# Kernel tuning notes

Measured on AMD Instinct MI355X. Metric: run time of the kernel, lower is better.

Reference implementation:

```python
import jax, jax.numpy as jnp
import numpy as np
import math

DIM_MODEL = 1024
N_HEAD = 16
NUM_NEURON = 64
MAX_LEN = 2048
B, S = 4, 2048


def setup_inputs() -> dict:
    key = jax.random.key(0)
    ks = jax.random.split(key, 11)
    d, p = DIM_MODEL, N_HEAD * NUM_NEURON
    sc_in = 1.0 / math.sqrt(d)
    sc_p = 1.0 / math.sqrt(p)
    return {
        "q": jax.random.normal(ks[0], (B, S, d), jnp.float32),
        "k": jax.random.normal(ks[1], (B, S, d), jnp.float32),
        "v": jax.random.normal(ks[2], (B, S, d), jnp.float32),
        "Wq": jax.random.normal(ks[3], (d, p), jnp.float32) * sc_in,
        "bq": jnp.zeros((p,), jnp.float32),
        "Wk": jax.random.normal(ks[4], (d, p), jnp.float32) * sc_in,
        "bk": jnp.zeros((p,), jnp.float32),
        "Wv": jax.random.normal(ks[5], (d, p), jnp.float32) * sc_in,
        "bv": jnp.zeros((p,), jnp.float32),
        "Wf": jax.random.normal(ks[6], (p, d), jnp.float32) * sc_p,
        "bf": jnp.zeros((d,), jnp.float32),
    }


def _split_heads(x):  # [B,S,H*Dh] -> [B,H,S,Dh]
    b, s, _ = x.shape
    return x.reshape(b, s, N_HEAD, NUM_NEURON).transpose(0, 2, 1, 3)


def reference(q, k, v, Wq, bq, Wk, bk, Wv, bv, Wf, bf):
    qh = _split_heads(q @ Wq + bq)
    kh = _split_heads(k @ Wk + bk)
    vh = _split_heads(v @ Wv + bv)
    # NOTE: original scales by 1/sqrt(max_len), not 1/sqrt(head_dim)
    scores = jnp.einsum("bhqd,bhkd->bhqk", qh, kh) / math.sqrt(MAX_LEN)
    s = scores.shape[-1]
    causal = jnp.tril(jnp.ones((s, s), bool))  # [S,S]
    scores = jnp.where(causal[None, None], scores, -jnp.inf)
    attn = jax.nn.softmax(scores, axis=-1)
    out = jnp.einsum("bhqk,bhkd->bhqd", attn, vh)  # [B,H,S,Dh]
    c = out.transpose(0, 2, 1, 3).reshape(out.shape[0], out.shape[2], N_HEAD * NUM_NEURON)
    return c @ Wf + bf
```

## Files before the change

### kernel.cpp

```cpp
#include <hip/hip_runtime.h>
#include <stdint.h>

#define DMODEL 1024
#define NHEAD 16
#define DH 64
#define BB 4
#define SS 2048
#define MROWS (BB * SS)

typedef __bf16 bfx8 __attribute__((ext_vector_type(8)));
typedef float f32x4 __attribute__((ext_vector_type(4)));
typedef float fvec4 __attribute__((ext_vector_type(4)));
typedef int i32x4 __attribute__((ext_vector_type(4)));
typedef unsigned short u16x8 __attribute__((ext_vector_type(8)));
typedef unsigned short u16x4 __attribute__((ext_vector_type(4)));

__device__ __forceinline__ unsigned short f2bf(float f) {
    union { float f; unsigned int u; } v; v.f = f;
    unsigned int r = v.u + 0x7FFFu + ((v.u >> 16) & 1u);
    return (unsigned short)(r >> 16);
}

__device__ __forceinline__ unsigned int cvtpk(float lo, float hi) {
    unsigned int r;
    asm("v_cvt_pk_bf16_f32 %0, %1, %2" : "=v"(r) : "v"(lo), "v"(hi));
    return r;
}

typedef __attribute__((address_space(1))) const void gas_t;
typedef __attribute__((address_space(3))) void las_t;
__device__ __forceinline__ void gload_lds16(const void* g, void* l) {
    __builtin_amdgcn_global_load_lds((gas_t*)g, (las_t*)l, 16, 0, 0);
}

__device__ __forceinline__ int sigma_k(int i) {
    return (i & 0x20) | ((i & 0x0C) << 1) | ((i & 0x10) >> 2) | (i & 3);
}

__global__ void cvt3_kernel(const float* __restrict__ s0, const float* __restrict__ s1,
                            const float* __restrict__ s2,
                            unsigned short* __restrict__ d0, unsigned short* __restrict__ d1,
                            unsigned short* __restrict__ d2, int n8)
{
    const float* s = (blockIdx.y == 0) ? s0 : (blockIdx.y == 1) ? s1 : s2;
    unsigned short* d = (blockIdx.y == 0) ? d0 : (blockIdx.y == 1) ? d1 : d2;
    int i = blockIdx.x * blockDim.x + threadIdx.x;
    if (i >= n8) return;
    fvec4 a = *reinterpret_cast<const fvec4*>(&s[(size_t)i * 8]);
    fvec4 b = *reinterpret_cast<const fvec4*>(&s[(size_t)i * 8 + 4]);
    u16x8 o;
    #pragma unroll
    for (int j = 0; j < 4; ++j) { o[j] = f2bf(a[j]); o[j + 4] = f2bf(b[j]); }
    *reinterpret_cast<u16x8*>(&d[(size_t)i * 8]) = o;
}

__global__ void transpose_cvt3_kernel(const float* __restrict__ W0, unsigned short* __restrict__ T0,
                                      const float* __restrict__ W1, unsigned short* __restrict__ T1,
                                      const float* __restrict__ W2, unsigned short* __restrict__ T2)
{
    const float* W = (blockIdx.z == 0) ? W0 : (blockIdx.z == 1) ? W1 : W2;
    unsigned short* Wt = (blockIdx.z == 0) ? T0 : (blockIdx.z == 1) ? T1 : T2;
    __shared__ unsigned short t[64][72];
    const int tid = threadIdx.x;
    const int r0 = blockIdx.y * 64, c0 = blockIdx.x * 64;
    #pragma unroll
    for (int i = 0; i < 4; ++i) {
        int idx = tid + i * 256;
        int r = idx >> 4, c4 = idx & 15;
        fvec4 v = *reinterpret_cast<const fvec4*>(&W[(size_t)(r0 + r) * DMODEL + c0 + c4 * 4]);
        #pragma unroll
        for (int j = 0; j < 4; ++j) t[c4 * 4 + j][r] = f2bf(v[j]);
    }
    __syncthreads();
    #pragma unroll
    for (int i = 0; i < 2; ++i) {
        int idx = tid + i * 256;
        int r = idx >> 3, c8 = idx & 7;
        u16x8 v = *reinterpret_cast<const u16x8*>(&t[r][c8 * 8]);
        *reinterpret_cast<u16x8*>(&Wt[(size_t)(c0 + r) * DMODEL + r0 + c8 * 8]) = v;
    }
}

struct GArg {
    const unsigned short* A;
    const unsigned short* Bt;
    const float* bias;
    void* O;
    float osc;
    int mode;
};

__global__ __launch_bounds__(256, 2)
void gemm_kernel(GArg g0, GArg g1, int M, int N, int K)
{
    const GArg g = blockIdx.z ? g1 : g0;
    __shared__ unsigned short sA[128 * 64];
    __shared__ unsigned short sB[128 * 64];
    const int tid  = threadIdx.x;
    const int lane = tid & 63;
    const int wave = tid >> 6;
    const int wm = (wave >> 1) * 64, wn = (wave & 1) * 64;
    const int m0 = blockIdx.x * 128, n0 = blockIdx.y * 128;
    const int lr = lane & 15;
    const int lg = lane >> 4;

    f32x4 acc[4][4] = {};

    for (int kk0 = 0; kk0 < K; kk0 += 64) {
        __syncthreads();
        #pragma unroll
        for (int i = 0; i < 4; ++i) {
            int c = tid + i * 256;
            int row = c >> 3, col8 = c & 7;
            gload_lds16(&g.A[(size_t)(m0 + row) * K + kk0 + col8 * 8], &sA[c * 8]);
        }
        #pragma unroll
        for (int i = 0; i < 4; ++i) {
            int c = tid + i * 256;
            int row = c >> 3, col8 = c & 7;
            gload_lds16(&g.Bt[(size_t)(n0 + row) * K + kk0 + col8 * 8], &sB[c * 8]);
        }
        __syncthreads();

        bfx8 af[4][2], bfr[4][2];
        #pragma unroll
        for (int m = 0; m < 4; ++m)
            #pragma unroll
            for (int kk = 0; kk < 2; ++kk)
                af[m][kk] = *reinterpret_cast<const bfx8*>(
                    &sA[(wm + m * 16 + lr) * 64 + kk * 32 + lg * 8]);
        #pragma unroll
        for (int n = 0; n < 4; ++n)
            #pragma unroll
            for (int kk = 0; kk < 2; ++kk)
                bfr[n][kk] = *reinterpret_cast<const bfx8*>(
                    &sB[(wn + n * 16 + lr) * 64 + kk * 32 + lg * 8]);
        #pragma unroll
        for (int kk = 0; kk < 2; ++kk)
            #pragma unroll
            for (int m = 0; m < 4; ++m)
                #pragma unroll
                for (int n = 0; n < 4; ++n)
                    acc[m][n] = __builtin_amdgcn_mfma_f32_16x16x32_bf16(
                        af[m][kk], bfr[n][kk], acc[m][n], 0, 0, 0);
    }

    #pragma unroll
    for (int n = 0; n < 4; ++n) {
        int col = n0 + wn + n * 16 + lr;
        float bv = g.bias[col];
        #pragma unroll
        for (int m = 0; m < 4; ++m) {
            int rowb = m0 + wm + m * 16 + lg * 4;
            float val[4];
            #pragma unroll
            for (int r = 0; r < 4; ++r) val[r] = (acc[m][n][r] + bv) * g.osc;
            if (g.mode == 0) {
                #pragma unroll
                for (int r = 0; r < 4; ++r)
                    ((unsigned short*)g.O)[(size_t)(rowb + r) * N + col] = f2bf(val[r]);
            } else if (g.mode == 2) {
                #pragma unroll
                for (int r = 0; r < 4; ++r)
                    ((float*)g.O)[(size_t)(rowb + r) * N + col] = val[r];
            } else {
                int bq = rowb >> 11, s = rowb & 2047;
                int hh = col >> 6, d = col & 63;
                u16x4 pk;
                #pragma unroll
                for (int r = 0; r < 4; ++r) pk[r] = f2bf(val[r]);
                size_t idx = ((size_t)(bq * 16 + hh) * 64 + d) * 2048 + s;
                *reinterpret_cast<u16x4*>(&((unsigned short*)g.O)[idx]) = pk;
            }
        }
    }
}

__global__ __launch_bounds__(256, 2)
void attn_kernel(const unsigned short* __restrict__ Q,
                 const unsigned short* __restrict__ K,
                 const unsigned short* __restrict__ Vt,
                 unsigned short* __restrict__ C)
{
    __shared__ unsigned short sK[64][72];
    __shared__ unsigned short sVt[64][72];

    const int tid  = threadIdx.x;
    const int lane = tid & 63;
    const int wave = tid >> 6;
    const int lr = lane & 15, lg = lane >> 4;
    const int bh = blockIdx.x;
    const int qt = (int)(gridDim.y - 1) - (int)blockIdx.y;
    const int b = bh >> 4, h = bh & 15;
    const int q0 = qt * 128;
    const size_t rowbase = (size_t)b * SS;
    const int hcol = h * DH;

    const int srow = tid >> 3, sc8 = tid & 7;
    const int sig0 = sigma_k(srow), sig1 = sigma_k(srow + 32);

    bfx8 aq[2][2];
    #pragma unroll
    for (int m = 0; m < 2; ++m) {
        int qr = q0 + wave * 32 + m * 16 + lr;
        const unsigned short* p = &Q[(rowbase + qr) * DMODEL + hcol + lg * 8];
        aq[m][0] = *reinterpret_cast<const bfx8*>(p);
        aq[m][1] = *reinterpret_cast<const bfx8*>(p + 32);
    }

    float m_run[2] = {0.f, 0.f};
    f32x4 l4[2] = {};
    f32x4 acc_o[2][4] = {};
    bool mz = true;
    const int qmax_wave = q0 + wave * 32 + 31;
    const int ntiles = 2 * qt + 2;

    for (int t = 0; t < ntiles; ++t) {
        const int k0 = t * 64;
        __syncthreads();
        *reinterpret_cast<u16x8*>(&sK[srow][sc8 * 8]) =
            *reinterpret_cast<const u16x8*>(
                &K[(rowbase + k0 + sig0) * DMODEL + hcol + sc8 * 8]);
        *reinterpret_cast<u16x8*>(&sK[srow + 32][sc8 * 8]) =
            *reinterpret_cast<const u16x8*>(
                &K[(rowbase + k0 + sig1) * DMODEL + hcol + sc8 * 8]);
        *reinterpret_cast<u16x8*>(&sVt[srow][sc8 * 8]) =
            *reinterpret_cast<const u16x8*>(
                &Vt[((size_t)bh * DH + srow) * SS + k0 + sc8 * 8]);
        *reinterpret_cast<u16x8*>(&sVt[srow + 32][sc8 * 8]) =
            *reinterpret_cast<const u16x8*>(
                &Vt[((size_t)bh * DH + srow + 32) * SS + k0 + sc8 * 8]);
        __syncthreads();
        if (k0 > qmax_wave) continue;

        f32x4 sc[2][4];
        __builtin_amdgcn_s_setprio(1);
        #pragma unroll
        for (int nf = 0; nf < 4; ++nf) {
            bfx8 ak0 = *reinterpret_cast<const bfx8*>(&sK[nf * 16 + lr][lg * 8]);
            bfx8 ak1 = *reinterpret_cast<const bfx8*>(&sK[nf * 16 + lr][32 + lg * 8]);
            #pragma unroll
            for (int m = 0; m < 2; ++m) {
                f32x4 s = {0.f, 0.f, 0.f, 0.f};
                s = __builtin_amdgcn_mfma_f32_16x16x32_bf16(ak0, aq[m][0], s, 0, 0, 0);
                s = __builtin_amdgcn_mfma_f32_16x16x32_bf16(ak1, aq[m][1], s, 0, 0, 0);
                sc[m][nf] = s;
            }
        }
        __builtin_amdgcn_s_setprio(0);
        #pragma unroll
        for (int m = 0; m < 2; ++m) {
            if (k0 + 63 > q0 + wave * 32 + m * 16) {
                int qrow = q0 + wave * 32 + m * 16 + lr;
                #pragma unroll
                for (int nf = 0; nf < 4; ++nf) {
                    int kb = k0 + ((nf >> 1) << 5) + (lg << 3) + ((nf & 1) << 2);
                    #pragma unroll
                    for (int r = 0; r < 4; ++r)
                        if (kb + r > qrow) sc[m][nf][r] = -3.0e38f;
                }
            }
        }
        f32x4 mx4 = sc[0][0];
        #pragma unroll
        for (int m = 0; m < 2; ++m)
            #pragma unroll
            for (int nf = 0; nf < 4; ++nf)
                #pragma unroll
                for (int r = 0; r < 4; ++r) mx4[r] = fmaxf(mx4[r], sc[m][nf][r]);
        float pmax = fmaxf(fmaxf(mx4[0], mx4[1]), fmaxf(mx4[2], mx4[3]));
        if (mz && __all(pmax <= 8.0f)) {
            #pragma unroll
            for (int m = 0; m < 2; ++m)
                #pragma unroll
                for (int nf = 0; nf < 4; ++nf) {
                    #pragma unroll
                    for (int r = 0; r < 4; ++r)
                        sc[m][nf][r] = __builtin_exp2f(sc[m][nf][r]);
                    l4[m] += sc[m][nf];
                }
        } else {
            mz = false;
            #pragma unroll
            for (int m = 0; m < 2; ++m) {
                float mx = -3.0e38f;
                #pragma unroll
                for (int nf = 0; nf < 4; ++nf)
                    #pragma unroll
                    for (int r = 0; r < 4; ++r) mx = fmaxf(mx, sc[m][nf][r]);
                mx = fmaxf(mx, __shfl_xor(mx, 16, 64));
                mx = fmaxf(mx, __shfl_xor(mx, 32, 64));
                float mnew = fmaxf(m_run[m], mx);
                float fs = __builtin_exp2f(m_run[m] - mnew);
                m_run[m] = mnew;
                f32x4 ps = {0.f, 0.f, 0.f, 0.f};
                #pragma unroll
                for (int nf = 0; nf < 4; ++nf) {
                    #pragma unroll
                    for (int r = 0; r < 4; ++r)
                        sc[m][nf][r] = __builtin_exp2f(sc[m][nf][r] - mnew);
                    ps += sc[m][nf];
                }
                #pragma unroll
                for (int r = 0; r < 4; ++r) l4[m][r] = l4[m][r] * fs + ps[r];
                #pragma unroll
                for (int r = 0; r < 4; ++r) {
                    float fsa = __shfl(fs, lg * 4 + r, 64);
                    #pragma unroll
                    for (int d = 0; d < 4; ++d) acc_o[m][d][r] *= fsa;
                }
            }
        }
        #pragma unroll
        for (int h2 = 0; h2 < 2; ++h2) {
            union { i32x4 i; bfx8 b; } pa[2];
            #pragma unroll
            for (int m = 0; m < 2; ++m) {
                pa[m].i[0] = cvtpk(sc[m][2 * h2][0],     sc[m][2 * h2][1]);
                pa[m].i[1] = cvtpk(sc[m][2 * h2][2],     sc[m][2 * h2][3]);
                pa[m].i[2] = cvtpk(sc[m][2 * h2 + 1][0], sc[m][2 * h2 + 1][1]);
                pa[m].i[3] = cvtpk(sc[m][2 * h2 + 1][2], sc[m][2 * h2 + 1][3]);
            }
            __builtin_amdgcn_s_setprio(1);
            #pragma unroll
            for (int d = 0; d < 4; ++d) {
                bfx8 bv0 = *reinterpret_cast<const bfx8*>(&sVt[d * 16 + lr][h2 * 32 + lg * 8]);
                acc_o[0][d] = __builtin_amdgcn_mfma_f32_16x16x32_bf16(pa[0].b, bv0, acc_o[0][d], 0, 0, 0);
                acc_o[1][d] = __builtin_amdgcn_mfma_f32_16x16x32_bf16(pa[1].b, bv0, acc_o[1][d], 0, 0, 0);
            }
            __builtin_amdgcn_s_setprio(0);
        }
    }

    #pragma unroll
    for (int m = 0; m < 2; ++m) {
        float l = (l4[m][0] + l4[m][1]) + (l4[m][2] + l4[m][3]);
        l += __shfl_xor(l, 16, 64);
        l += __shfl_xor(l, 32, 64);
        float linv = 1.0f / l;
        float linva[4];
        #pragma unroll
        for (int r = 0; r < 4; ++r) linva[r] = __shfl(linv, lg * 4 + r, 64);
        const int qrb = q0 + wave * 32 + m * 16 + lg * 4;
        #pragma unroll
        for (int d = 0; d < 4; ++d) {
            int col = hcol + d * 16 + lr;
            #pragma unroll
            for (int r = 0; r < 4; ++r)
                C[(rowbase + qrb + r) * DMODEL + col] = f2bf(acc_o[m][d][r] * linva[r]);
        }
    }
}

extern "C" void kernel_launch(void* const* d_in, const int* in_sizes, int n_in,
                              void* d_out, int out_size, void* d_ws, size_t ws_size,
                              hipStream_t stream)
{
    const float* q  = (const float*)d_in[0];
    const float* k  = (const float*)d_in[1];
    const float* v  = (const float*)d_in[2];
    const float* Wq = (const float*)d_in[3];
    const float* bq = (const float*)d_in[4];
    const float* Wk = (const float*)d_in[5];
    const float* bk = (const float*)d_in[6];
    const float* Wv = (const float*)d_in[7];
    const float* bv = (const float*)d_in[8];
    const float* Wf = (const float*)d_in[9];
    const float* bf = (const float*)d_in[10];

    unsigned short* ws = (unsigned short*)d_ws;
    const size_t SZ = (size_t)MROWS * DMODEL;
    unsigned short* ws0 = ws;
    unsigned short* ws1 = ws + SZ;
    unsigned short* ws2 = ws + 2 * SZ;
    unsigned short* ws3 = ws + 3 * SZ;

    unsigned short* scr = (unsigned short*)d_out;
    unsigned short* WqT = scr;
    unsigned short* WkT = scr + 1048576;
    unsigned short* WvT = scr + 2097152;
    unsigned short* Qb  = scr + 4194304;

    const float qscale = 0.02209708691207961f * 1.44269504088896341f;

    const int n8 = (int)(SZ / 8);
    cvt3_kernel<<<dim3((n8 + 255) / 256, 3), 256, 0, stream>>>(q, k, v, ws0, ws1, ws2, n8);

    transpose_cvt3_kernel<<<dim3(16, 16, 3), 256, 0, stream>>>(Wq, WqT, Wk, WkT, Wv, WvT);

    {
        GArg gq{ws0, WqT, bq, Qb,  qscale, 0};
        GArg gk{ws1, WkT, bk, ws3, 1.0f,   0};
        gemm_kernel<<<dim3(64, 8, 2), 256, 0, stream>>>(gq, gk, MROWS, DMODEL, DMODEL);
    }
    {
        GArg gv{ws2, WvT, bv, ws0, 1.0f, 3};
        gemm_kernel<<<dim3(64, 8, 1), 256, 0, stream>>>(gv, gv, MROWS, DMODEL, DMODEL);
    }
    transpose_cvt3_kernel<<<dim3(16, 16, 1), 256, 0, stream>>>(Wf, ws2, Wf, ws2, Wf, ws2);

    attn_kernel<<<dim3(BB * NHEAD, SS / 128), 256, 0, stream>>>(Qb, ws3, ws0, ws1);

    {
        GArg gf{ws1, ws2, bf, (float*)d_out, 1.0f, 2};
        gemm_kernel<<<dim3(64, 8, 1), 256, 0, stream>>>(gf, gf, MROWS, DMODEL, DMODEL);
    }
}
```

Before: 212.8 us.

## Prefetch next K/V tile into registers and XOR-swizzle shared memory layout

The attention kernel now loads the next K and Vt tile from global memory into registers while the current tile is being computed, then stores them to shared memory at the top of the next iteration. This is meant to hide global load latency behind the MFMA work. The padded shared arrays are replaced with unpadded 64x64 arrays using an XOR swizzle on the 16-byte chunk index, to avoid bank conflicts without the padding. It costs extra registers for the prefetch buffers, which could reduce occupancy under launch_bounds(256,2).

```diff
diff --git a/kernel.cpp b/kernel.cpp
--- a/kernel.cpp
+++ b/kernel.cpp
@@ -182,8 +182,8 @@
                  const unsigned short* __restrict__ Vt,
                  unsigned short* __restrict__ C)
 {
-    __shared__ unsigned short sK[64][72];
-    __shared__ unsigned short sVt[64][72];
+    __shared__ unsigned short sK[64 * 64];
+    __shared__ unsigned short sV[64 * 64];
 
     const int tid  = threadIdx.x;
     const int lane = tid & 63;
@@ -198,6 +198,9 @@
 
     const int srow = tid >> 3, sc8 = tid & 7;
     const int sig0 = sigma_k(srow), sig1 = sigma_k(srow + 32);
+    const int woff0 = srow * 64 + ((sc8 ^ (srow & 7)) * 8);
+    const int woff1 = (srow + 32) * 64 + ((sc8 ^ (srow & 7)) * 8);
+    const int p0 = lg ^ (lr & 7);
 
     bfx8 aq[2][2];
     #pragma unroll
@@ -215,30 +218,38 @@
     const int qmax_wave = q0 + wave * 32 + 31;
     const int ntiles = 2 * qt + 2;
 
+    u16x8 rk0, rk1, rv0, rv1;
+    {
+        rk0 = *reinterpret_cast<const u16x8*>(&K[(rowbase + 0 + sig0) * DMODEL + hcol + sc8 * 8]);
+        rk1 = *reinterpret_cast<const u16x8*>(&K[(rowbase + 0 + sig1) * DMODEL + hcol + sc8 * 8]);
+        rv0 = *reinterpret_cast<const u16x8*>(&Vt[((size_t)bh * DH + srow) * SS + 0 + sc8 * 8]);
+        rv1 = *reinterpret_cast<const u16x8*>(&Vt[((size_t)bh * DH + srow + 32) * SS + 0 + sc8 * 8]);
+    }
+
     for (int t = 0; t < ntiles; ++t) {
+        __syncthreads();
+        *reinterpret_cast<u16x8*>(&sK[woff0]) = rk0;
+        *reinterpret_cast<u16x8*>(&sK[woff1]) = rk1;
+        *reinterpret_cast<u16x8*>(&sV[woff0]) = rv0;
+        *reinterpret_cast<u16x8*>(&sV[woff1]) = rv1;
+        __syncthreads();
+        if (t + 1 < ntiles) {
+            const int kk = (t + 1) * 64;
+            rk0 = *reinterpret_cast<const u16x8*>(&K[(rowbase + kk + sig0) * DMODEL + hcol + sc8 * 8]);
+            rk1 = *reinterpret_cast<const u16x8*>(&K[(rowbase + kk + sig1) * DMODEL + hcol + sc8 * 8]);
+            rv0 = *reinterpret_cast<const u16x8*>(&Vt[((size_t)bh * DH + srow) * SS + kk + sc8 * 8]);
+            rv1 = *reinterpret_cast<const u16x8*>(&Vt[((size_t)bh * DH + srow + 32) * SS + kk + sc8 * 8]);
+        }
         const int k0 = t * 64;
-        __syncthreads();
-        *reinterpret_cast<u16x8*>(&sK[srow][sc8 * 8]) =
-            *reinterpret_cast<const u16x8*>(
-                &K[(rowbase + k0 + sig0) * DMODEL + hcol + sc8 * 8]);
-        *reinterpret_cast<u16x8*>(&sK[srow + 32][sc8 * 8]) =
-            *reinterpret_cast<const u16x8*>(
-                &K[(rowbase + k0 + sig1) * DMODEL + hcol + sc8 * 8]);
-        *reinterpret_cast<u16x8*>(&sVt[srow][sc8 * 8]) =
-            *reinterpret_cast<const u16x8*>(
-                &Vt[((size_t)bh * DH + srow) * SS + k0 + sc8 * 8]);
-        *reinterpret_cast<u16x8*>(&sVt[srow + 32][sc8 * 8]) =
-            *reinterpret_cast<const u16x8*>(
-                &Vt[((size_t)bh * DH + srow + 32) * SS + k0 + sc8 * 8]);
-        __syncthreads();
         if (k0 > qmax_wave) continue;
 
         f32x4 sc[2][4];
         __builtin_amdgcn_s_setprio(1);
         #pragma unroll
         for (int nf = 0; nf < 4; ++nf) {
-            bfx8 ak0 = *reinterpret_cast<const bfx8*>(&sK[nf * 16 + lr][lg * 8]);
-            bfx8 ak1 = *reinterpret_cast<const bfx8*>(&sK[nf * 16 + lr][32 + lg * 8]);
+            int i = nf * 16 + lr;
+            bfx8 ak0 = *reinterpret_cast<const bfx8*>(&sK[i * 64 + p0 * 8]);
+            bfx8 ak1 = *reinterpret_cast<const bfx8*>(&sK[i * 64 + (p0 ^ 4) * 8]);
             #pragma unroll
             for (int m = 0; m < 2; ++m) {
                 f32x4 s = {0.f, 0.f, 0.f, 0.f};
@@ -324,7 +335,9 @@
             __builtin_amdgcn_s_setprio(1);
             #pragma unroll
             for (int d = 0; d < 4; ++d) {
-                bfx8 bv0 = *reinterpret_cast<const bfx8*>(&sVt[d * 16 + lr][h2 * 32 + lg * 8]);
+                int i = d * 16 + lr;
+                int pv = ((h2 << 2) | lg) ^ (lr & 7);
+                bfx8 bv0 = *reinterpret_cast<const bfx8*>(&sV[i * 64 + pv * 8]);
                 acc_o[0][d] = __builtin_amdgcn_mfma_f32_16x16x32_bf16(pa[0].b, bv0, acc_o[0][d], 0, 0, 0);
                 acc_o[1][d] = __builtin_amdgcn_mfma_f32_16x16x32_bf16(pa[1].b, bv0, acc_o[1][d], 0, 0, 0);
             }
```

Measured after the change: 213.6 us. No clear change (+0.4%).
